# Kernel tuning notes

Measured on AMD Instinct MI355X. Metric: run time of the kernel, lower is better.

Reference implementation:

```python
import jax, jax.numpy as jnp
import numpy as np

ALPHA = 0.2
MASK_VAL = -9e15
LN_EPS = 1e-5

def leaky(x):
    return jnp.where(x >= 0, x, ALPHA * x)

def setup_inputs() -> dict:
    key = jax.random.key(0)
    ks = jax.random.split(key, 8)
    B, N, D = 4, 4096, 128
    x = jax.random.normal(ks[0], (B, N, D), dtype=jnp.float32)
    adj = jax.random.randint(ks[1], (N, N), 0, 2, dtype=jnp.int32)
    W = jax.random.normal(ks[2], (D, D), dtype=jnp.float32) * (2.0 / D) ** 0.5
    a1 = jax.random.normal(ks[3], (D, 1), dtype=jnp.float32) * (1.0 / D) ** 0.5
    a2 = jax.random.normal(ks[4], (D, 1), dtype=jnp.float32) * (1.0 / D) ** 0.5
    node_weights = jax.random.normal(ks[5], (N,), dtype=jnp.float32)
    node_bias = jnp.zeros((N,), dtype=jnp.float32)
    gamma = jnp.ones((D,), dtype=jnp.float32)
    beta = jnp.zeros((D,), dtype=jnp.float32)
    return {"x": x, "adj": adj, "W": W, "a1": a1, "a2": a2,
            "node_weights": node_weights, "node_bias": node_bias,
            "gamma": gamma, "beta": beta}

def reference(x, adj, W, a1, a2, node_weights, node_bias, gamma, beta):
    # node-wise affine + residual (dropout is identity in eval mode)
    res = x
    x = x * node_weights[None, :, None] + node_bias[None, :, None] + res  # [B,N,D]
    # linear projection + LayerNorm
    h = jnp.matmul(x, W)  # [B,N,D]
    mu = jnp.mean(h, axis=-1, keepdims=True)
    var = jnp.mean((h - mu) ** 2, axis=-1, keepdims=True)
    h = (h - mu) / jnp.sqrt(var + LN_EPS) * gamma + beta
    residential = h
    # GAT-style additive scores: e[b,i,j] = leakyrelu(f1[b,i] + f2[b,j])
    f1 = jnp.matmul(h, a1)[..., 0]  # [B,N]
    f2 = jnp.matmul(h, a2)[..., 0]  # [B,N]
    e = leaky(f1[:, :, None] + f2[:, None, :])  # [B,N,N]
    # adjacency masking (no softmax in original), second leakyrelu
    att = jnp.where(adj[None] > 0, e, MASK_VAL)
    att = leaky(att)
    h_prime = jnp.matmul(att, h)  # [B,N,D]
    return jax.nn.elu(h_prime) + residential
```

## Files before the change

### kernel.cpp

```cpp
#include <hip/hip_runtime.h>
#include <hip/hip_bf16.h>

typedef short bfrag8 __attribute__((ext_vector_type(8)));
typedef float f32x4v __attribute__((ext_vector_type(4)));
typedef int i32x4 __attribute__((ext_vector_type(4)));
typedef unsigned short U16;
typedef unsigned int U32;

#define NN 4096
#define DD 128

static __device__ __forceinline__ U16 f2bf(float f){
  union { __hip_bfloat16 b; U16 u; } cv;
  cv.b = __float2bfloat16(f);
  return cv.u;
}

static __device__ __forceinline__ float bf2f(U32 u){
  union { float f; U32 u; } cv;
  cv.u = u << 16;
  return cv.f;
}

static __device__ __forceinline__ i32x4 afragi8(U32 wl, U32 wh, int grp, U32 mul){
  U32 y = ((grp & 2) ? wh : wl) >> ((grp & 1) * 16);
  i32x4 a;
  a[0] = (int)((((y >>  0) & 0xFu) * mul) & 0x01010101u);
  a[1] = (int)((((y >>  4) & 0xFu) * mul) & 0x01010101u);
  a[2] = (int)((((y >>  8) & 0xFu) * mul) & 0x01010101u);
  a[3] = (int)((((y >> 12) & 0xFu) * mul) & 0x01010101u);
  return a;
}

__global__ __launch_bounds__(256) void k0_combo(const int* __restrict__ adj,
                                                U32* __restrict__ adjbT,
                                                const float* __restrict__ W,
                                                U16* __restrict__ WT){
  if (blockIdx.x >= 2048){
    int i = (blockIdx.x - 2048)*256 + threadIdx.x;
    int d = i >> 7, dp = i & 127;
    WT[dp*128 + d] = f2bf(W[i]);
    return;
  }
  const int g   = blockIdx.x >> 4;
  const int row = (blockIdx.x & 15)*256 + threadIdx.x;
  const int4* src = reinterpret_cast<const int4*>(adj + (size_t)row*NN + g*32);
  int4 v[8];
  #pragma unroll
  for (int c = 0; c < 8; ++c) v[c] = src[c];
  U32 m = 0;
  #pragma unroll
  for (int c = 0; c < 8; ++c){
    m |= (v[c].x != 0 ? 0u : 1u) << (c*4);
    m |= (v[c].y != 0 ? 0u : 2u) << (c*4);
    m |= (v[c].z != 0 ? 0u : 4u) << (c*4);
    m |= (v[c].w != 0 ? 0u : 8u) << (c*4);
  }
  adjbT[(size_t)g*4096 + row] = m;
}

__global__ __launch_bounds__(512) void k1_prep(
    const float* __restrict__ x, const U16* __restrict__ WT,
    const float* __restrict__ nw, const float* __restrict__ nb,
    const float* __restrict__ gamma, const float* __restrict__ beta,
    U16* __restrict__ h_lnB, char* __restrict__ hTi8)
{
  __shared__ char smem[66560];
  U16* lds = reinterpret_cast<U16*>(smem);
  float4* xs4 = reinterpret_cast<float4*>(smem + 32768);
  float2* lnx = reinterpret_cast<float2*>(smem + 65536);
  const int tid = threadIdx.x;
  const int lane = tid & 63, w = tid >> 6;
  const int rh = w >> 1, ch = w & 1;
  const int l15 = lane & 15, grp = lane >> 4;

  #pragma unroll
  for (int q = 0; q < 4; ++q){
    int cid = q*512 + tid;
    int dp = cid >> 4, c = cid & 15;
    *reinterpret_cast<int4*>(lds + dp*128 + ((c*8) ^ ((dp&15)<<3))) =
        *reinterpret_cast<const int4*>(WT + cid*8);
  }
  {
    const float4* xg = reinterpret_cast<const float4*>(x) + (size_t)blockIdx.x*2048;
    #pragma unroll
    for (int k = 0; k < 4; ++k){
      int g = k*512 + tid;
      int row = g >> 5, c = g & 31;
      xs4[row*32 + ((c + row*2) & 31)] = xg[g];
    }
  }
  __syncthreads();

  const int rA = blockIdx.x*64 + rh*16 + l15;
  const int nA = rA & 4095;
  const float wgt = nw[nA] + 1.0f, bia = nb[nA];
  const int xrow = rh*16 + l15;

  f32x4v acc[4] = {};
  #pragma unroll
  for (int ks = 0; ks < 4; ++ks){
    int c0 = ks*8 + grp*2;
    float4 xa = xs4[xrow*32 + ((c0     + xrow*2) & 31)];
    float4 xb = xs4[xrow*32 + ((c0 + 1 + xrow*2) & 31)];
    bfrag8 af;
    af[0] = (short)f2bf(xa.x*wgt + bia);
    af[1] = (short)f2bf(xa.y*wgt + bia);
    af[2] = (short)f2bf(xa.z*wgt + bia);
    af[3] = (short)f2bf(xa.w*wgt + bia);
    af[4] = (short)f2bf(xb.x*wgt + bia);
    af[5] = (short)f2bf(xb.y*wgt + bia);
    af[6] = (short)f2bf(xb.z*wgt + bia);
    af[7] = (short)f2bf(xb.w*wgt + bia);
    #pragma unroll
    for (int nf = 0; nf < 4; ++nf){
      int dp = ch*64 + nf*16 + l15;
      bfrag8 bf = *reinterpret_cast<const bfrag8*>(
          lds + dp*128 + ((((ks*4 + grp)*8)) ^ ((dp&15)<<3)));
      acc[nf] = __builtin_amdgcn_mfma_f32_16x16x32_bf16(af, bf, acc[nf], 0, 0, 0);
    }
  }

  #pragma unroll
  for (int r = 0; r < 4; ++r){
    float s = 0.f, qq = 0.f;
    #pragma unroll
    for (int nf = 0; nf < 4; ++nf){ float v = acc[nf][r]; s += v; qq += v*v; }
    #pragma unroll
    for (int m = 1; m < 16; m <<= 1){ s += __shfl_xor(s, m); qq += __shfl_xor(qq, m); }
    if (l15 == 0) lnx[ch*64 + rh*16 + grp*4 + r] = make_float2(s, qq);
  }
  __syncthreads();

  float gc[4], bc[4];
  #pragma unroll
  for (int nf = 0; nf < 4; ++nf){
    int col = ch*64 + nf*16 + l15;
    gc[nf] = gamma[col]; bc[nf] = beta[col];
  }

  #pragma unroll
  for (int r = 0; r < 4; ++r){
    const int lrow = rh*16 + grp*4 + r;
    float2 pa = lnx[lrow], pb = lnx[64 + lrow];
    float s = pa.x + pb.x, qq = pa.y + pb.y;
    float mu = s * 0.0078125f;
    float var = fmaxf(qq*0.0078125f - mu*mu, 0.f);
    float rstd = rsqrtf(var + 1e-5f);
    const int rC = blockIdx.x*64 + lrow;
    #pragma unroll
    for (int nf = 0; nf < 4; ++nf){
      float hn = (acc[nf][r] - mu)*rstd*gc[nf] + bc[nf];
      acc[nf][r] = hn;
      h_lnB[(size_t)rC*DD + ch*64 + nf*16 + l15] = f2bf(hn);
    }
  }

  __syncthreads();
  #pragma unroll
  for (int r = 0; r < 4; ++r)
    #pragma unroll
    for (int nf = 0; nf < 4; ++nf)
      lds[(rh*16 + grp*4 + r)*128 + ch*64 + nf*16 + l15] = f2bf(acc[nf][r]);
  __syncthreads();

  {
    const int r0 = blockIdx.x*64;
    const int bB = r0 >> 12;
    const int nt = (r0 & 4095) >> 6;
    char* dstt = hTi8 + (((size_t)(bB*64 + nt)*128) << 6);
    const int d = tid & 127, q4 = tid >> 7;
    int pk[4];
    #pragma unroll
    for (int j = 0; j < 4; ++j){
      U32 word = 0;
      #pragma unroll
      for (int c = 0; c < 4; ++c){
        float v = bf2f((U32)lds[(q4*16 + j*4 + c)*128 + d]);
        float qf = fminf(fmaxf(rintf(v*32.f), -127.f), 127.f);
        int qi = (int)qf;
        word |= ((U32)(qi & 0xFF)) << (c*8);
      }
      pk[j] = (int)word;
    }
    int4 pa; pa.x = pk[0]; pa.y = pk[1]; pa.z = pk[2]; pa.w = pk[3];
    *reinterpret_cast<int4*>(dstt + (size_t)d*64 + q4*16) = pa;
  }
}

__global__ __launch_bounds__(512, 2) void k2_main(
    const U32* __restrict__ adjbT, const char* __restrict__ hTi8,
    const U16* __restrict__ h_lnB, float* __restrict__ out)
{
  __shared__ int part[32768];
  const int tid = threadIdx.x;
  const int lane = tid & 63, w = tid >> 6;
  const int l15 = lane & 15, grp = lane >> 4;
  const int bid = blockIdx.x;
  const int xcd = bid & 7;
  const int b = xcd >> 1;
  const int iblk = (((bid >> 3) << 1) | (xcd & 1)) * 64;
  const float CM2 = 0.2f * -9.0e15f / 32.0f;
  const U32 MUL = 0x00204081u;

  const U32* ar0 = adjbT + (size_t)(w*16)*4096 + iblk +      l15;
  const U32* ar1 = adjbT + (size_t)(w*16)*4096 + iblk + 16 + l15;
  const U32* ar2 = adjbT + (size_t)(w*16)*4096 + iblk + 32 + l15;
  const U32* ar3 = adjbT + (size_t)(w*16)*4096 + iblk + 48 + l15;

  const char* bp = hTi8 + (((size_t)(b*64 + w*8)*128) << 6) + l15*64 + grp*16;

  i32x4 acc[4][8] = {};

#define LOADB(P0,P1,P2,P3,P4,P5,P6,P7, S) do { \
    const char* _q = bp + (size_t)(S)*8192; \
    P0 = *reinterpret_cast<const i32x4*>(_q);        \
    P1 = *reinterpret_cast<const i32x4*>(_q + 1024); \
    P2 = *reinterpret_cast<const i32x4*>(_q + 2048); \
    P3 = *reinterpret_cast<const i32x4*>(_q + 3072); \
    P4 = *reinterpret_cast<const i32x4*>(_q + 4096); \
    P5 = *reinterpret_cast<const i32x4*>(_q + 5120); \
    P6 = *reinterpret_cast<const i32x4*>(_q + 6144); \
    P7 = *reinterpret_cast<const i32x4*>(_q + 7168); } while(0)

#define LOADW(L0,H0,L1,H1,L2,H2,L3,H3, S) do { \
    L0 = ar0[(size_t)(2*(S))*4096];   H0 = ar0[(size_t)(2*(S)+1)*4096]; \
    L1 = ar1[(size_t)(2*(S))*4096];   H1 = ar1[(size_t)(2*(S)+1)*4096]; \
    L2 = ar2[(size_t)(2*(S))*4096];   H2 = ar2[(size_t)(2*(S)+1)*4096]; \
    L3 = ar3[(size_t)(2*(S))*4096];   H3 = ar3[(size_t)(2*(S)+1)*4096]; } while(0)

#define COLM(CF, NF) do { \
    acc[0][NF] = __builtin_amdgcn_mfma_i32_16x16x64_i8(a0, CF, acc[0][NF], 0,0,0); \
    acc[1][NF] = __builtin_amdgcn_mfma_i32_16x16x64_i8(a1, CF, acc[1][NF], 0,0,0); \
    acc[2][NF] = __builtin_amdgcn_mfma_i32_16x16x64_i8(a2, CF, acc[2][NF], 0,0,0); \
    acc[3][NF] = __builtin_amdgcn_mfma_i32_16x16x64_i8(a3, CF, acc[3][NF], 0,0,0); } while(0)

#define COMPUTE(P0,P1,P2,P3,P4,P5,P6,P7, L0,H0,L1,H1,L2,H2,L3,H3) do { \
    i32x4 a0 = afragi8(L0, H0, grp, MUL); \
    i32x4 a1 = afragi8(L1, H1, grp, MUL); \
    i32x4 a2 = afragi8(L2, H2, grp, MUL); \
    i32x4 a3 = afragi8(L3, H3, grp, MUL); \
    COLM(P0, 0); COLM(P1, 1); COLM(P2, 2); COLM(P3, 3); \
    COLM(P4, 4); COLM(P5, 5); COLM(P6, 6); COLM(P7, 7); } while(0)

  i32x4 A0,A1,A2,A3,A4,A5,A6,A7, B0,B1,B2,B3,B4,B5,B6,B7;
  U32 aL0,aH0,aL1,aH1,aL2,aH2,aL3,aH3;
  U32 bL0,bH0,bL1,bH1,bL2,bH2,bL3,bH3;

  LOADB(A0,A1,A2,A3,A4,A5,A6,A7, 0);
  LOADW(aL0,aH0,aL1,aH1,aL2,aH2,aL3,aH3, 0);

  #pragma unroll 1
  for (int it = 0; it < 4; ++it){
    const int s = it*2;
    LOADB(B0,B1,B2,B3,B4,B5,B6,B7, s+1);
    LOADW(bL0,bH0,bL1,bH1,bL2,bH2,bL3,bH3, s+1);
    COMPUTE(A0,A1,A2,A3,A4,A5,A6,A7, aL0,aH0,aL1,aH1,aL2,aH2,aL3,aH3);
    LOADB(A0,A1,A2,A3,A4,A5,A6,A7, s+2);
    LOADW(aL0,aH0,aL1,aH1,aL2,aH2,aL3,aH3, s+2);
    COMPUTE(B0,B1,B2,B3,B4,B5,B6,B7, bL0,bH0,bL1,bH1,bL2,bH2,bL3,bH3);
  }

  {
    int* reg = part + (w & 3)*8192;
    if (w < 4){
      #pragma unroll
      for (int f = 0; f < 4; ++f)
        #pragma unroll
        for (int nf = 0; nf < 8; ++nf){
          const int col = nf*16 + l15;
          #pragma unroll
          for (int r = 0; r < 4; ++r){
            const int lr = f*16 + grp*4 + r;
            reg[lr*128 + (col ^ (((lr>>2)&3)<<4))] = acc[f][nf][r];
          }
        }
    }
    __syncthreads();
    if (w >= 4){
      #pragma unroll
      for (int f = 0; f < 4; ++f)
        #pragma unroll
        for (int nf = 0; nf < 8; ++nf){
          const int col = nf*16 + l15;
          #pragma unroll
          for (int r = 0; r < 4; ++r){
            const int lr = f*16 + grp*4 + r;
            const int idx = lr*128 + (col ^ (((lr>>2)&3)<<4));
            reg[idx] += acc[f][nf][r];
          }
        }
    }
    __syncthreads();
  }

  #pragma unroll
  for (int rr = 0; rr < 8; ++rr){
    const int row = w*8 + rr;
    const int sw = ((row>>2)&3)<<4;
    const int idx = row*128 + ((2*lane) ^ sw);
    int s0 = 0, s1 = 0;
    #pragma unroll
    for (int q = 0; q < 4; ++q){
      int2 v = *reinterpret_cast<const int2*>(part + q*8192 + idx);
      s0 += v.x; s1 += v.y;
    }
    const float h0 = CM2 * (float)s0, h1 = CM2 * (float)s1;
    const float e0 = h0 > 0.f ? h0 : __expf(h0) - 1.f;
    const float e1 = h1 > 0.f ? h1 : __expf(h1) - 1.f;
    const size_t o = ((size_t)b*NN + iblk + row)*DD + 2*lane;
    const U32 hl = *reinterpret_cast<const U32*>(h_lnB + o);
    float2 ov; ov.x = e0 + bf2f(hl & 0xffffu); ov.y = e1 + bf2f(hl >> 16);
    *reinterpret_cast<float2*>(out + o) = ov;
  }
#undef COLM
#undef COMPUTE
#undef LOADW
#undef LOADB
}

extern "C" void kernel_launch(void* const* d_in, const int* in_sizes, int n_in,
                              void* d_out, int out_size, void* d_ws, size_t ws_size,
                              hipStream_t stream) {
  const float* x     = (const float*)d_in[0];
  const int*   adj   = (const int*)  d_in[1];
  const float* W     = (const float*)d_in[2];
  const float* nw    = (const float*)d_in[5];
  const float* nb    = (const float*)d_in[6];
  const float* gamma = (const float*)d_in[7];
  const float* beta  = (const float*)d_in[8];
  float* out = (float*)d_out;

  char* ws = (char*)d_ws;
  U16*  h_lnB = (U16*)(ws);
  char* hTi8  = (char*)(ws + 4*1024*1024);
  U16*  WT    = (U16*)(ws + 6*1024*1024 + 64*1024);
  U32*  adjbT = (U32*)(ws + 7*1024*1024);

  k0_combo<<<dim3(2112), dim3(256), 0, stream>>>(adj, adjbT, W, WT);
  k1_prep <<<dim3(256),  dim3(512), 0, stream>>>(x, WT, nw, nb, gamma, beta,
                                                 h_lnB, hTi8);
  k2_main <<<dim3(256),  dim3(512), 0, stream>>>(adjbT, hTi8, h_lnB, out);
}
```

Measured before the change: 43.04 us.

## Split k2_main waves over column halves to halve accumulators and LDS

Each wave now covers half of the 128 output columns and twice as many K steps, instead of all 128 columns. This halves the per-wave accumulator and B-fragment registers and halves the LDS reduction buffer. The launch bound rises to 4 blocks per CU for more occupancy. In exchange, the adjacency A-fragments are loaded and unpacked twice, once per column-half wave, so unpacking work and adjacency traffic per block go up.

```diff
diff --git a/kernel.cpp b/kernel.cpp
--- a/kernel.cpp
+++ b/kernel.cpp
@@ -188,13 +188,14 @@
   }
 }
 
-__global__ __launch_bounds__(512, 2) void k2_main(
+__global__ __launch_bounds__(512, 4) void k2_main(
     const U32* __restrict__ adjbT, const char* __restrict__ hTi8,
     const U16* __restrict__ h_lnB, float* __restrict__ out)
 {
-  __shared__ int part[32768];
+  __shared__ int part[16384];
   const int tid = threadIdx.x;
   const int lane = tid & 63, w = tid >> 6;
+  const int ch = w & 1, kq = w >> 1;
   const int l15 = lane & 15, grp = lane >> 4;
   const int bid = blockIdx.x;
   const int xcd = bid & 7;
@@ -203,31 +204,26 @@
   const float CM2 = 0.2f * -9.0e15f / 32.0f;
   const U32 MUL = 0x00204081u;
 
-  const U32* ar0 = adjbT + (size_t)(w*16)*4096 + iblk +      l15;
-  const U32* ar1 = adjbT + (size_t)(w*16)*4096 + iblk + 16 + l15;
-  const U32* ar2 = adjbT + (size_t)(w*16)*4096 + iblk + 32 + l15;
-  const U32* ar3 = adjbT + (size_t)(w*16)*4096 + iblk + 48 + l15;
-
-  const char* bp = hTi8 + (((size_t)(b*64 + w*8)*128) << 6) + l15*64 + grp*16;
-
-  i32x4 acc[4][8] = {};
-
-#define LOADB(P0,P1,P2,P3,P4,P5,P6,P7, S) do { \
+  const U32* ar = adjbT + (size_t)(kq*32)*4096 + iblk + l15;
+  const char* bp = hTi8 + (((size_t)(b*64 + kq*16)*128 + ch*64) << 6)
+                   + l15*64 + grp*16;
+
+  i32x4 acc[4][4] = {};
+
+#define LOADB(P0,P1,P2,P3, S) do { \
     const char* _q = bp + (size_t)(S)*8192; \
     P0 = *reinterpret_cast<const i32x4*>(_q);        \
     P1 = *reinterpret_cast<const i32x4*>(_q + 1024); \
     P2 = *reinterpret_cast<const i32x4*>(_q + 2048); \
-    P3 = *reinterpret_cast<const i32x4*>(_q + 3072); \
-    P4 = *reinterpret_cast<const i32x4*>(_q + 4096); \
-    P5 = *reinterpret_cast<const i32x4*>(_q + 5120); \
-    P6 = *reinterpret_cast<const i32x4*>(_q + 6144); \
-    P7 = *reinterpret_cast<const i32x4*>(_q + 7168); } while(0)
+    P3 = *reinterpret_cast<const i32x4*>(_q + 3072); } while(0)
 
 #define LOADW(L0,H0,L1,H1,L2,H2,L3,H3, S) do { \
-    L0 = ar0[(size_t)(2*(S))*4096];   H0 = ar0[(size_t)(2*(S)+1)*4096]; \
-    L1 = ar1[(size_t)(2*(S))*4096];   H1 = ar1[(size_t)(2*(S)+1)*4096]; \
-    L2 = ar2[(size_t)(2*(S))*4096];   H2 = ar2[(size_t)(2*(S)+1)*4096]; \
-    L3 = ar3[(size_t)(2*(S))*4096];   H3 = ar3[(size_t)(2*(S)+1)*4096]; } while(0)
+    const U32* _a = ar + (size_t)(2*(S))*4096; \
+    const U32* _b = ar + (size_t)(2*(S)+1)*4096; \
+    L0 = _a[0];  H0 = _b[0]; \
+    L1 = _a[16]; H1 = _b[16]; \
+    L2 = _a[32]; H2 = _b[32]; \
+    L3 = _a[48]; H3 = _b[48]; } while(0)
 
 #define COLM(CF, NF) do { \
     acc[0][NF] = __builtin_amdgcn_mfma_i32_16x16x64_i8(a0, CF, acc[0][NF], 0,0,0); \
@@ -235,40 +231,39 @@
     acc[2][NF] = __builtin_amdgcn_mfma_i32_16x16x64_i8(a2, CF, acc[2][NF], 0,0,0); \
     acc[3][NF] = __builtin_amdgcn_mfma_i32_16x16x64_i8(a3, CF, acc[3][NF], 0,0,0); } while(0)
 
-#define COMPUTE(P0,P1,P2,P3,P4,P5,P6,P7, L0,H0,L1,H1,L2,H2,L3,H3) do { \
+#define COMPUTE(P0,P1,P2,P3, L0,H0,L1,H1,L2,H2,L3,H3) do { \
     i32x4 a0 = afragi8(L0, H0, grp, MUL); \
     i32x4 a1 = afragi8(L1, H1, grp, MUL); \
     i32x4 a2 = afragi8(L2, H2, grp, MUL); \
     i32x4 a3 = afragi8(L3, H3, grp, MUL); \
-    COLM(P0, 0); COLM(P1, 1); COLM(P2, 2); COLM(P3, 3); \
-    COLM(P4, 4); COLM(P5, 5); COLM(P6, 6); COLM(P7, 7); } while(0)
-
-  i32x4 A0,A1,A2,A3,A4,A5,A6,A7, B0,B1,B2,B3,B4,B5,B6,B7;
+    COLM(P0, 0); COLM(P1, 1); COLM(P2, 2); COLM(P3, 3); } while(0)
+
+  i32x4 A0,A1,A2,A3, B0,B1,B2,B3;
   U32 aL0,aH0,aL1,aH1,aL2,aH2,aL3,aH3;
   U32 bL0,bH0,bL1,bH1,bL2,bH2,bL3,bH3;
 
-  LOADB(A0,A1,A2,A3,A4,A5,A6,A7, 0);
+  LOADB(A0,A1,A2,A3, 0);
   LOADW(aL0,aH0,aL1,aH1,aL2,aH2,aL3,aH3, 0);
 
   #pragma unroll 1
-  for (int it = 0; it < 4; ++it){
+  for (int it = 0; it < 8; ++it){
     const int s = it*2;
-    LOADB(B0,B1,B2,B3,B4,B5,B6,B7, s+1);
+    LOADB(B0,B1,B2,B3, s+1);
     LOADW(bL0,bH0,bL1,bH1,bL2,bH2,bL3,bH3, s+1);
-    COMPUTE(A0,A1,A2,A3,A4,A5,A6,A7, aL0,aH0,aL1,aH1,aL2,aH2,aL3,aH3);
-    LOADB(A0,A1,A2,A3,A4,A5,A6,A7, s+2);
+    COMPUTE(A0,A1,A2,A3, aL0,aH0,aL1,aH1,aL2,aH2,aL3,aH3);
+    LOADB(A0,A1,A2,A3, s+2);
     LOADW(aL0,aH0,aL1,aH1,aL2,aH2,aL3,aH3, s+2);
-    COMPUTE(B0,B1,B2,B3,B4,B5,B6,B7, bL0,bH0,bL1,bH1,bL2,bH2,bL3,bH3);
+    COMPUTE(B0,B1,B2,B3, bL0,bH0,bL1,bH1,bL2,bH2,bL3,bH3);
   }
 
   {
-    int* reg = part + (w & 3)*8192;
-    if (w < 4){
+    int* reg = part + (kq & 1)*8192;
+    if (kq < 2){
       #pragma unroll
       for (int f = 0; f < 4; ++f)
         #pragma unroll
-        for (int nf = 0; nf < 8; ++nf){
-          const int col = nf*16 + l15;
+        for (int nf = 0; nf < 4; ++nf){
+          const int col = ch*64 + nf*16 + l15;
           #pragma unroll
           for (int r = 0; r < 4; ++r){
             const int lr = f*16 + grp*4 + r;
@@ -277,12 +272,12 @@
         }
     }
     __syncthreads();
-    if (w >= 4){
+    if (kq >= 2){
       #pragma unroll
       for (int f = 0; f < 4; ++f)
         #pragma unroll
-        for (int nf = 0; nf < 8; ++nf){
-          const int col = nf*16 + l15;
+        for (int nf = 0; nf < 4; ++nf){
+          const int col = ch*64 + nf*16 + l15;
           #pragma unroll
           for (int r = 0; r < 4; ++r){
             const int lr = f*16 + grp*4 + r;
@@ -299,12 +294,9 @@
     const int row = w*8 + rr;
     const int sw = ((row>>2)&3)<<4;
     const int idx = row*128 + ((2*lane) ^ sw);
-    int s0 = 0, s1 = 0;
-    #pragma unroll
-    for (int q = 0; q < 4; ++q){
-      int2 v = *reinterpret_cast<const int2*>(part + q*8192 + idx);
-      s0 += v.x; s1 += v.y;
-    }
+    int2 v0 = *reinterpret_cast<const int2*>(part + idx);
+    int2 v1 = *reinterpret_cast<const int2*>(part + 8192 + idx);
+    const int s0 = v0.x + v1.x, s1 = v0.y + v1.y;
     const float h0 = CM2 * (float)s0, h1 = CM2 * (float)s1;
     const float e0 = h0 > 0.f ? h0 : __expf(h0) - 1.f;
     const float e1 = h1 > 0.f ? h1 : __expf(h1) - 1.f;
```

Result: no change. 43.10 us (+0.1%).
